# Kernel optimization log

Measured on AMD Instinct MI355X. Metric: run time of the kernel, lower is better.

The kernel has to match this reference:

```python
import jax, jax.numpy as jnp
import numpy as np

ALPHA = 0.2  # LeakyReLU negative slope


def setup_inputs() -> dict:
    key = jax.random.key(0)
    ks = jax.random.split(key, 6)
    B, N, F_in, F_out, H = 16, 1024, 256, 256, 8
    h = jax.random.normal(ks[0], (B, N, F_in), dtype=jnp.float32)
    # Per-head Linear W: weight [F_out, F_in] + bias [F_out], stacked over heads
    W = jax.random.normal(ks[1], (H, F_out, F_in), dtype=jnp.float32) * (1.414 / np.sqrt(F_in))
    bW = jax.random.normal(ks[2], (H, F_out), dtype=jnp.float32) * 0.01
    # Per-head Linear A: weight [1, 2*F_out] split into a1 (acts on Whi) and a2 (acts on Whj), bias bA [1]
    a1 = jax.random.normal(ks[3], (H, F_out), dtype=jnp.float32) * (1.414 / np.sqrt(2 * F_out))
    a2 = jax.random.normal(ks[4], (H, F_out), dtype=jnp.float32) * (1.414 / np.sqrt(2 * F_out))
    bA = jax.random.normal(ks[5], (H,), dtype=jnp.float32) * 0.01
    return {"h": h, "W": W, "bW": bW, "a1": a1, "a2": a2, "bA": bA}


def reference(h, W, bW, a1, a2, bA):
    # h: [B,N,F_in], W: [H,F_out,F_in]
    B, N, _ = h.shape
    H, F_out, _ = W.shape
    Wh = jnp.einsum('bnf,hof->bhno', h, W) + bW[None, :, None, :]  # [B,H,N,F_out]
    # Additive score e_ij = a1.Wh_i + a2.Wh_j + bA  (decomposed; avoids N x N x 2F concat)
    ei = jnp.einsum('bhno,ho->bhn', Wh, a1)  # contribution of row node i
    ej = jnp.einsum('bhno,ho->bhn', Wh, a2)  # contribution of col node j
    e = ei[:, :, :, None] + ej[:, :, None, :] + bA[None, :, None, None]  # [B,H,N,N]
    e = jnp.where(e > 0, e, ALPHA * e)  # LeakyReLU
    att = jax.nn.softmax(e, axis=-1)  # softmax over neighbors j (dropout = identity in eval)
    aWh = jnp.einsum('bhij,bhjo->bhio', att, Wh)  # [B,H,N,F_out]
    out = jax.nn.relu(aWh)  # last=False branch
    out = out.transpose(0, 2, 1, 3).reshape(B, N, H * F_out)  # concat heads on feature dim
    return jax.nn.sigmoid(out)
```

## Files before the change

### kernel.cpp

```cpp
#include <hip/hip_runtime.h>


#define L2E 1.442695041f

typedef _Float16 half8 __attribute__((ext_vector_type(8)));
typedef __fp16 fp16x2 __attribute__((ext_vector_type(2)));
typedef float floatx4 __attribute__((ext_vector_type(4)));

#if __has_builtin(__builtin_amdgcn_exp2f)
#define EXP2F(x) __builtin_amdgcn_exp2f(x)
#else
#define EXP2F(x) exp2f(x)
#endif

static __device__ inline unsigned int pack2(float a, float b) {
    fp16x2 h = __builtin_amdgcn_cvt_pkrtz(a, b);
    return __builtin_bit_cast(unsigned int, h);
}

typedef __attribute__((address_space(1))) const void GV;
typedef __attribute__((address_space(3))) void LV;
static __device__ inline void load_lds16(const void* g, void* l) {
    __builtin_amdgcn_global_load_lds((GV*)g, (LV*)l, 16, 0, 0);
}

static __device__ inline int swz(int row, int c) {
    return (row << 6) + ((((c) ^ (row >> 1)) & 3) << 4);
}
static __device__ inline int swz128(int row, int c) {
    return (row << 7) + ((((c) ^ row) & 7) << 4);
}

__global__ __launch_bounds__(256, 3) void wh_kernel(
    const float* __restrict__ hin, const float* __restrict__ W,
    const float* __restrict__ bW, _Float16* __restrict__ WhT,
    const float* __restrict__ a1, const float* __restrict__ a2,
    float* __restrict__ eiP, float* __restrict__ ejP)
{
    const int bnt  = blockIdx.x;
    const int ot   = blockIdx.y;
    const int head = blockIdx.z;
    const int t    = threadIdx.x;
    const int wave = t >> 6, lane = t & 63;
    const int l15 = lane & 15, quad = lane >> 4;
    const int wmh = wave & 1, wnh = wave >> 1;

    __shared__ char smem[16384];
    _Float16* As = (_Float16*)smem;
    _Float16* Bs = (_Float16*)(smem + 8192);
    float* bWs   = (float*)smem;
    float* a1s   = (float*)(smem + 512);
    float* a2s   = (float*)(smem + 1024);
    float* part1 = (float*)(smem + 1536);
    float* part2 = (float*)(smem + 2560);

    const int o0 = ot * 128;
    const int bn0 = bnt * 128;
    floatx4 acc[4][4];
#pragma unroll
    for (int a = 0; a < 4; a++)
#pragma unroll
        for (int b = 0; b < 4; b++) acc[a][b] = (floatx4)0.0f;

    const int ar = t >> 1, ah = t & 1;
    const float* Wrow = W + (size_t)(head * 256 + o0 + ar) * 256 + ah * 16;
    const float* hrow = hin + (size_t)(bn0 + ar) * 256 + ah * 16;

    float4 pa0, pa1, pa2, pa3, pb0, pb1, pb2, pb3;
    {
        const float4* p4 = (const float4*)Wrow;
        pa0 = p4[0]; pa1 = p4[1]; pa2 = p4[2]; pa3 = p4[3];
        const float4* q4 = (const float4*)hrow;
        pb0 = q4[0]; pb1 = q4[1]; pb2 = q4[2]; pb3 = q4[3];
    }

    for (int f0 = 0; f0 < 256; f0 += 32) {
        __syncthreads();
        *(uint4*)((char*)As + swz(ar, 2 * ah)) =
            make_uint4(pack2(pa0.x, pa0.y), pack2(pa0.z, pa0.w),
                       pack2(pa1.x, pa1.y), pack2(pa1.z, pa1.w));
        *(uint4*)((char*)As + swz(ar, 2 * ah + 1)) =
            make_uint4(pack2(pa2.x, pa2.y), pack2(pa2.z, pa2.w),
                       pack2(pa3.x, pa3.y), pack2(pa3.z, pa3.w));
        *(uint4*)((char*)Bs + swz(ar, 2 * ah)) =
            make_uint4(pack2(pb0.x, pb0.y), pack2(pb0.z, pb0.w),
                       pack2(pb1.x, pb1.y), pack2(pb1.z, pb1.w));
        *(uint4*)((char*)Bs + swz(ar, 2 * ah + 1)) =
            make_uint4(pack2(pb2.x, pb2.y), pack2(pb2.z, pb2.w),
                       pack2(pb3.x, pb3.y), pack2(pb3.z, pb3.w));
        if (f0 < 224) {
            const float4* p4 = (const float4*)(Wrow + f0 + 32);
            pa0 = p4[0]; pa1 = p4[1]; pa2 = p4[2]; pa3 = p4[3];
            const float4* q4 = (const float4*)(hrow + f0 + 32);
            pb0 = q4[0]; pb1 = q4[1]; pb2 = q4[2]; pb3 = q4[3];
        }
        __syncthreads();
        half8 af[4], bf[4];
#pragma unroll
        for (int a = 0; a < 4; a++)
            af[a] = *(const half8*)((char*)As + swz(wmh * 64 + a * 16 + l15, quad));
#pragma unroll
        for (int b = 0; b < 4; b++)
            bf[b] = *(const half8*)((char*)Bs + swz(wnh * 64 + b * 16 + l15, quad));
#pragma unroll
        for (int a = 0; a < 4; a++)
#pragma unroll
            for (int b = 0; b < 4; b++)
                acc[a][b] = __builtin_amdgcn_mfma_f32_16x16x32_f16(af[a], bf[b], acc[a][b], 0, 0, 0);
    }

    __syncthreads();
    if (t < 128) {
        bWs[t] = bW[head * 256 + o0 + t];
        a1s[t] = a1[head * 256 + o0 + t];
        a2s[t] = a2[head * 256 + o0 + t];
    }
    __syncthreads();

    const int bidx = bn0 >> 10;
    const int nbase = bn0 & 1023;
#pragma unroll
    for (int b = 0; b < 4; b++) {
        const int bnl = wnh * 64 + b * 16 + l15;
        const int n = nbase + bnl;
        float p1 = 0.f, p2 = 0.f;
#pragma unroll
        for (int a = 0; a < 4; a++) {
#pragma unroll
            for (int r = 0; r < 4; r++) {
                int ol = wmh * 64 + a * 16 + quad * 4 + r;
                float v = acc[a][b][r] + bWs[ol];
                WhT[(((size_t)(bidx * 8 + head) * 256 + o0 + ol) << 10) + n] = (_Float16)v;
                p1 = fmaf(v, a1s[ol], p1);
                p2 = fmaf(v, a2s[ol], p2);
            }
        }
        p1 += __shfl_xor(p1, 16, 64); p1 += __shfl_xor(p1, 32, 64);
        p2 += __shfl_xor(p2, 16, 64); p2 += __shfl_xor(p2, 32, 64);
        if (lane < 16) {
            part1[wmh * 128 + bnl] = p1;
            part2[wmh * 128 + bnl] = p2;
        }
    }
    __syncthreads();
    if (t < 128) {
        float s1 = part1[t] + part1[128 + t];
        float s2 = part2[t] + part2[128 + t];
        const size_t idx = (size_t)(bidx * 8 + head) * 1024 + nbase + t;
        eiP[(size_t)ot * 131072 + idx] = s1;
        ejP[(size_t)ot * 131072 + idx] = s2;
    }
}

__global__ __launch_bounds__(256, 2) void pv_kernel(
    const _Float16* __restrict__ WhT, const float* __restrict__ eiP,
    const float* __restrict__ ejP, const float* __restrict__ bA,
    float* __restrict__ out)
{
    const int bh = blockIdx.x;
    const int it = blockIdx.y;
    const int b = bh >> 3, head = bh & 7;
    const int t = threadIdx.x;
    const int wave = t >> 6, lane = t & 63;
    const int l15 = lane & 15, quad = lane >> 4;
    const int wmh = wave & 1, wnh = wave >> 1;

    __shared__ char smem[53776];
    _Float16* Ap = (_Float16*)smem;
    _Float16* Bp = (_Float16*)(smem + 16384);
    float* ejs  = (float*)(smem + 49152);
    float* lns  = (float*)(smem + 53248);
    float* wred = (float*)(smem + 53760);

    const float* ej0 = ejP + bh * 1024;
    const float* ej1 = ejP + 131072 + bh * 1024;
    float mx = -1e30f;
#pragma unroll
    for (int k = 0; k < 4; k++) {
        int idx = t + k * 256;
        float v = (ej0[idx] + ej1[idx]) * L2E;
        ejs[idx] = v;
        mx = fmaxf(mx, v);
    }
#pragma unroll
    for (int m = 32; m; m >>= 1) mx = fmaxf(mx, __shfl_xor(mx, m, 64));
    if (lane == 0) wred[wave] = mx;
    __syncthreads();
    float ejmax = fmaxf(fmaxf(wred[0], wred[1]), fmaxf(wred[2], wred[3]));

    const int i0 = it * 128;
    const int prow = t >> 1, pjh = t & 1;
    const float cip = (eiP[bh * 1024 + i0 + prow] +
                       eiP[131072 + bh * 1024 + i0 + prow] + bA[head]) * L2E;
    const float tmv = cip + ejmax;
    const float nm = -fmaxf(tmv, 0.2f * tmv);

    const int rsub = lane >> 3, cp7 = lane & 7;
    const _Float16* bsrc = WhT + ((size_t)bh << 18)
                         + ((size_t)(wave * 64 + rsub) << 10)
                         + ((cp7 ^ rsub) << 3);
    char* bdst0 = (char*)Bp + wave * 8192;

    floatx4 acc[4][8], accl[4];
#pragma unroll
    for (int a = 0; a < 4; a++) {
        accl[a] = (floatx4)0.0f;
#pragma unroll
        for (int c = 0; c < 8; c++) acc[a][c] = (floatx4)0.0f;
    }
    const bool doL = (wnh == 0);
    const half8 ones = {1, 1, 1, 1, 1, 1, 1, 1};

    for (int j0 = 0; j0 < 1024; j0 += 64) {
        __syncthreads();
#pragma unroll
        for (int q = 0; q < 8; q++)
            load_lds16(bsrc + j0 + q * 8192, bdst0 + q * 1024);
        {
            const float4* ejp4 = (const float4*)(ejs + j0 + pjh * 32);
#pragma unroll
            for (int q = 0; q < 4; q++) {
                float4 e4a = ejp4[2 * q], e4b = ejp4[2 * q + 1];
                float p[8];
                const float ev[8] = {e4a.x, e4a.y, e4a.z, e4a.w,
                                     e4b.x, e4b.y, e4b.z, e4b.w};
#pragma unroll
                for (int u = 0; u < 8; u++) {
                    float e = cip + ev[u];
                    float lr = fmaxf(e, 0.2f * e);
                    p[u] = EXP2F(lr + nm);
                }
                *(uint4*)((char*)Ap + swz128(prow, pjh * 4 + q)) =
                    make_uint4(pack2(p[0], p[1]), pack2(p[2], p[3]),
                               pack2(p[4], p[5]), pack2(p[6], p[7]));
            }
        }
        __syncthreads();
#pragma unroll
        for (int kk = 0; kk < 2; kk++) {
            half8 af[4], bf[8];
#pragma unroll
            for (int a = 0; a < 4; a++)
                af[a] = *(const half8*)((char*)Ap + swz128(wmh * 64 + a * 16 + l15, kk * 4 + quad));
#pragma unroll
            for (int c = 0; c < 8; c++)
                bf[c] = *(const half8*)((char*)Bp + swz128(wnh * 128 + c * 16 + l15, kk * 4 + quad));
            if (doL) {
#pragma unroll
                for (int a = 0; a < 4; a++)
                    accl[a] = __builtin_amdgcn_mfma_f32_16x16x32_f16(af[a], ones, accl[a], 0, 0, 0);
            }
#pragma unroll
            for (int a = 0; a < 4; a++)
#pragma unroll
                for (int c = 0; c < 8; c++)
                    acc[a][c] = __builtin_amdgcn_mfma_f32_16x16x32_f16(af[a], bf[c], acc[a][c], 0, 0, 0);
        }
    }

    __syncthreads();
    if (doL && l15 == 0) {
#pragma unroll
        for (int a = 0; a < 4; a++)
#pragma unroll
            for (int r = 0; r < 4; r++)
                lns[wmh * 64 + a * 16 + quad * 4 + r] = accl[a][r];
    }
    __syncthreads();

    float rinv[4][4];
#pragma unroll
    for (int a = 0; a < 4; a++)
#pragma unroll
        for (int r = 0; r < 4; r++)
            rinv[a][r] = 1.0f / lns[wmh * 64 + a * 16 + quad * 4 + r];

#pragma unroll
    for (int a = 0; a < 4; a++) {
#pragma unroll
        for (int c = 0; c < 8; c++) {
            int o = wnh * 128 + c * 16 + l15;
#pragma unroll
            for (int r = 0; r < 4; r++) {
                int i = i0 + wmh * 64 + a * 16 + quad * 4 + r;
                float v = acc[a][c][r] * rinv[a][r];
                float rl = fmaxf(v, 0.0f);
                float y = 1.0f / (1.0f + EXP2F(-rl * L2E));
                out[((size_t)(b * 1024 + i) << 11) + head * 256 + o] = y;
            }
        }
    }
}

extern "C" void kernel_launch(void* const* d_in, const int* in_sizes, int n_in,
                              void* d_out, int out_size, void* d_ws, size_t ws_size,
                              hipStream_t stream)
{
    const float* h  = (const float*)d_in[0];
    const float* W  = (const float*)d_in[1];
    const float* bW = (const float*)d_in[2];
    const float* a1 = (const float*)d_in[3];
    const float* a2 = (const float*)d_in[4];
    const float* bA = (const float*)d_in[5];
    float* out = (float*)d_out;

    char* ws = (char*)d_ws;
    _Float16* WhT = (_Float16*)ws;
    float* eiP = (float*)(ws + 67108864);
    float* ejP = (float*)(ws + 67108864 + 1048576);

    hipLaunchKernelGGL(wh_kernel, dim3(128, 2, 8), dim3(256), 0, stream,
                       h, W, bW, WhT, a1, a2, eiP, ejP);
    hipLaunchKernelGGL(pv_kernel, dim3(128, 8), dim3(256), 0, stream,
                       WhT, eiP, ejP, bA, out);
}
```

Before: 280.8 us.

## Double-buffer WhT tiles with 32-wide K steps and manual waitcnt pipelining in pv_kernel

Restructures the pv_kernel main loop to use 32-column j tiles with a double-buffered B tile in LDS. The next WhT tile is prefetched via global_load_lds while probabilities for the current tile are generated, with explicit vmcnt/lgkmcnt waits and barriers in place of two __syncthreads per 64-column step. LDS footprint drops, which may allow higher occupancy, and setprio raises priority around the MFMA block. The cost is twice as many loop iterations and barriers, and a fragile hand-written waitcnt schedule.

Measured after the change: 287.5 us. +2.4%, slower.

```diff
diff --git a/kernel.cpp b/kernel.cpp
--- a/kernel.cpp
+++ b/kernel.cpp
@@ -26,9 +26,6 @@
 
 static __device__ inline int swz(int row, int c) {
     return (row << 6) + ((((c) ^ (row >> 1)) & 3) << 4);
-}
-static __device__ inline int swz128(int row, int c) {
-    return (row << 7) + ((((c) ^ row) & 7) << 4);
 }
 
 __global__ __launch_bounds__(256, 3) void wh_kernel(
@@ -165,12 +162,12 @@
     const int l15 = lane & 15, quad = lane >> 4;
     const int wmh = wave & 1, wnh = wave >> 1;
 
-    __shared__ char smem[53776];
+    __shared__ char smem[45584];
     _Float16* Ap = (_Float16*)smem;
-    _Float16* Bp = (_Float16*)(smem + 16384);
-    float* ejs  = (float*)(smem + 49152);
-    float* lns  = (float*)(smem + 53248);
-    float* wred = (float*)(smem + 53760);
+    char* BpB   = smem + 8192;
+    float* ejs  = (float*)(smem + 40960);
+    float* lns  = (float*)(smem + 45056);
+    float* wred = (float*)(smem + 45568);
 
     const float* ej0 = ejP + bh * 1024;
     const float* ej1 = ejP + 131072 + bh * 1024;
@@ -195,11 +192,11 @@
     const float tmv = cip + ejmax;
     const float nm = -fmaxf(tmv, 0.2f * tmv);
 
-    const int rsub = lane >> 3, cp7 = lane & 7;
+    const int rsub = lane >> 2, cpos = lane & 3, perm = (lane >> 3) & 3;
     const _Float16* bsrc = WhT + ((size_t)bh << 18)
                          + ((size_t)(wave * 64 + rsub) << 10)
-                         + ((cp7 ^ rsub) << 3);
-    char* bdst0 = (char*)Bp + wave * 8192;
+                         + ((cpos ^ perm) << 3);
+    char* bdst = BpB + wave * 4096;
 
     floatx4 acc[4][8], accl[4];
 #pragma unroll
@@ -211,52 +208,73 @@
     const bool doL = (wnh == 0);
     const half8 ones = {1, 1, 1, 1, 1, 1, 1, 1};
 
-    for (int j0 = 0; j0 < 1024; j0 += 64) {
-        __syncthreads();
-#pragma unroll
-        for (int q = 0; q < 8; q++)
-            load_lds16(bsrc + j0 + q * 8192, bdst0 + q * 1024);
-        {
-            const float4* ejp4 = (const float4*)(ejs + j0 + pjh * 32);
-#pragma unroll
-            for (int q = 0; q < 4; q++) {
-                float4 e4a = ejp4[2 * q], e4b = ejp4[2 * q + 1];
-                float p[8];
-                const float ev[8] = {e4a.x, e4a.y, e4a.z, e4a.w,
-                                     e4b.x, e4b.y, e4b.z, e4b.w};
-#pragma unroll
-                for (int u = 0; u < 8; u++) {
-                    float e = cip + ev[u];
-                    float lr = fmaxf(e, 0.2f * e);
-                    p[u] = EXP2F(lr + nm);
-                }
-                *(uint4*)((char*)Ap + swz128(prow, pjh * 4 + q)) =
-                    make_uint4(pack2(p[0], p[1]), pack2(p[2], p[3]),
-                               pack2(p[4], p[5]), pack2(p[6], p[7]));
+    auto pgen = [&](int j0) {
+        const float4* ejp4 = (const float4*)(ejs + j0 + pjh * 16);
+#pragma unroll
+        for (int q = 0; q < 2; q++) {
+            float4 e4a = ejp4[2 * q], e4b = ejp4[2 * q + 1];
+            float p[8];
+            const float ev[8] = {e4a.x, e4a.y, e4a.z, e4a.w,
+                                 e4b.x, e4b.y, e4b.z, e4b.w};
+#pragma unroll
+            for (int u = 0; u < 8; u++) {
+                float e = cip + ev[u];
+                float lr = fmaxf(e, 0.2f * e);
+                p[u] = EXP2F(lr + nm);
             }
-        }
-        __syncthreads();
-#pragma unroll
-        for (int kk = 0; kk < 2; kk++) {
-            half8 af[4], bf[8];
+            *(uint4*)((char*)Ap + swz(prow, pjh * 2 + q)) =
+                make_uint4(pack2(p[0], p[1]), pack2(p[2], p[3]),
+                           pack2(p[4], p[5]), pack2(p[6], p[7]));
+        }
+    };
+
+    auto mstep = [&](const char* Bcur) {
+        half8 af[4], bf[8];
+#pragma unroll
+        for (int a = 0; a < 4; a++)
+            af[a] = *(const half8*)((char*)Ap + swz(wmh * 64 + a * 16 + l15, quad));
+#pragma unroll
+        for (int c = 0; c < 8; c++)
+            bf[c] = *(const half8*)(Bcur + swz(wnh * 128 + c * 16 + l15, quad));
+        __builtin_amdgcn_s_setprio(1);
+        if (doL) {
 #pragma unroll
             for (int a = 0; a < 4; a++)
-                af[a] = *(const half8*)((char*)Ap + swz128(wmh * 64 + a * 16 + l15, kk * 4 + quad));
+                accl[a] = __builtin_amdgcn_mfma_f32_16x16x32_f16(af[a], ones, accl[a], 0, 0, 0);
+        }
+#pragma unroll
+        for (int a = 0; a < 4; a++)
 #pragma unroll
             for (int c = 0; c < 8; c++)
-                bf[c] = *(const half8*)((char*)Bp + swz128(wnh * 128 + c * 16 + l15, kk * 4 + quad));
-            if (doL) {
-#pragma unroll
-                for (int a = 0; a < 4; a++)
-                    accl[a] = __builtin_amdgcn_mfma_f32_16x16x32_f16(af[a], ones, accl[a], 0, 0, 0);
-            }
-#pragma unroll
-            for (int a = 0; a < 4; a++)
-#pragma unroll
-                for (int c = 0; c < 8; c++)
-                    acc[a][c] = __builtin_amdgcn_mfma_f32_16x16x32_f16(af[a], bf[c], acc[a][c], 0, 0, 0);
-        }
-    }
+                acc[a][c] = __builtin_amdgcn_mfma_f32_16x16x32_f16(af[a], bf[c], acc[a][c], 0, 0, 0);
+        __builtin_amdgcn_s_setprio(0);
+    };
+
+#pragma unroll
+    for (int q = 0; q < 4; q++)
+        load_lds16(bsrc + q * 16384, bdst + q * 1024);
+
+#pragma unroll 2
+    for (int tt = 0; tt < 31; ++tt) {
+        const int nb = (tt + 1) & 1;
+#pragma unroll
+        for (int q = 0; q < 4; q++)
+            load_lds16(bsrc + (tt + 1) * 32 + q * 16384,
+                       bdst + nb * 16384 + q * 1024);
+        pgen(tt * 32);
+        asm volatile("s_waitcnt vmcnt(4) lgkmcnt(0)" ::: "memory");
+        asm volatile("s_barrier" ::: "memory");
+        __builtin_amdgcn_sched_barrier(0);
+        mstep(BpB + (tt & 1) * 16384);
+        asm volatile("s_waitcnt lgkmcnt(0)" ::: "memory");
+        asm volatile("s_barrier" ::: "memory");
+        __builtin_amdgcn_sched_barrier(0);
+    }
+    pgen(31 * 32);
+    asm volatile("s_waitcnt vmcnt(0) lgkmcnt(0)" ::: "memory");
+    asm volatile("s_barrier" ::: "memory");
+    __builtin_amdgcn_sched_barrier(0);
+    mstep(BpB + 16384);
 
     __syncthreads();
     if (doL && l15 == 0) {
```
